# Optimization experiments

Hardware: AMD Instinct MI355X
Metric: run time of the kernel (lower is better)

The kernel has to match this reference:

```python
import jax, jax.numpy as jnp
import numpy as np

N_BATCH, C, H, W = 4, 64, 64, 64


def setup_inputs() -> dict:
    key = jax.random.key(0)
    ks = jax.random.split(key, 8)
    x = jax.random.normal(ks[0], (N_BATCH, C, H, W), dtype=jnp.float32)
    wb = jax.random.normal(ks[1], (C, C), dtype=jnp.float32) * 0.05
    bb = jax.random.normal(ks[2], (C,), dtype=jnp.float32) * 0.05
    wc = jax.random.normal(ks[3], (C, C), dtype=jnp.float32) * 0.05
    bc = jax.random.normal(ks[4], (C,), dtype=jnp.float32) * 0.05
    wd = jax.random.normal(ks[5], (C, C), dtype=jnp.float32) * 0.05
    bd = jax.random.normal(ks[6], (C,), dtype=jnp.float32) * 0.05
    alpha = jax.random.normal(ks[7], (1,), dtype=jnp.float32)
    return {"x": x, "wb": wb, "bb": bb, "wc": wc, "bc": bc,
            "wd": wd, "bd": bd, "alpha": alpha}


def reference(x, wb, bb, wc, bc, wd, bd, alpha):
    n, c, h, w = x.shape
    xf = x.reshape(n, c, h * w)  # (n, c, L)
    # 1x1 convs == per-pixel channel GEMMs
    xb = jnp.einsum('oc,ncl->nol', wb, xf) + bb[None, :, None]  # keys   (n, c, L)
    xc = jnp.einsum('oc,ncl->nol', wc, xf) + bc[None, :, None]  # queries(n, c, L)
    xd = jnp.einsum('oc,ncl->nol', wd, xf) + bd[None, :, None]  # values (n, c, L)
    # attention[i, j] = <xc[:, i], xb[:, j]>, softmax over j
    attention = jnp.einsum('nci,ncj->nij', xc, xb)  # (n, L, L)
    att = jax.nn.softmax(attention, axis=-1)
    # x_o[:, :, i] = sum_j xd[:, :, j] * att[i, j]
    x_o = jnp.einsum('ncj,nij->nci', xd, att).reshape(n, c, h, w)
    return alpha[0] * x_o + x
```

## Files before the change

### kernel.cpp

```cpp
#include <hip/hip_runtime.h>
#include <hip/hip_bf16.h>

typedef unsigned short u16;
typedef unsigned char u8;
typedef unsigned int u32;
typedef long long i64;
typedef __attribute__((ext_vector_type(4))) float f32x4;
typedef __attribute__((ext_vector_type(4))) unsigned int u32x4;

#define L_SEQ 4096
#define NCH 64
#define NBATCH 4
#define NW 8
#define KVSPAN (L_SEQ / NW)
#define QB 32
#define DEFER_THR 4.0f

__device__ inline u16 f2bf(float f) {
    union { float f; u32 u; } v; v.f = f;
    u32 r = v.u + 0x7fffu + ((v.u >> 16) & 1u);
    return (u16)(r >> 16);
}

template <bool WORD>
__device__ inline u32 pk_fp8(float a, float b, u32 old) {
    return (u32)__builtin_amdgcn_cvt_pk_fp8_f32(a, b, (int)old, WORD);
}
__device__ inline u8 fp8_1(float a) {
    return (u8)(__builtin_amdgcn_cvt_pk_fp8_f32(a, a, 0, false) & 0xff);
}

__global__ __launch_bounds__(256) void qkv_kernel(
    const float* __restrict__ x,
    const float* __restrict__ wb, const float* __restrict__ bb,
    const float* __restrict__ wc, const float* __restrict__ bc,
    const float* __restrict__ wd, const float* __restrict__ bd,
    u8* __restrict__ Qp8, u8* __restrict__ Kp8, u8* __restrict__ Vp8)
{
    __shared__ float xs[64][64];
    __shared__ float wl[3][64][65];

    const int nb  = blockIdx.y;
    const int i0  = blockIdx.x * 64;
    const int tid = threadIdx.x;

    const float* xbase = x + (size_t)nb * NCH * L_SEQ + i0;
    #pragma unroll
    for (int rep = 0; rep < 16; ++rep) {
        int idx = rep * 256 + tid;
        int c = idx >> 6, px = idx & 63;
        xs[c][px] = xbase[(size_t)c * L_SEQ + px];
    }
    const float* wsrc[3] = { wb, wc, wd };
    for (int m = 0; m < 3; ++m) {
        #pragma unroll
        for (int rep = 0; rep < 16; ++rep) {
            int idx = rep * 256 + tid;
            wl[m][idx >> 6][idx & 63] = wsrc[m][idx];
        }
    }
    __syncthreads();

    const int co  = tid & 63;
    const int pg  = tid >> 6;
    const int px0 = pg * 16;

    float accB[16], accC[16], accD[16];
    const float biasB = bb[co], biasC = bc[co], biasD = bd[co];
    #pragma unroll
    for (int p = 0; p < 16; ++p) { accB[p] = biasB; accC[p] = biasC; accD[p] = biasD; }

    for (int c = 0; c < 64; ++c) {
        const float wbv = wl[0][co][c];
        const float wcv = wl[1][co][c];
        const float wdv = wl[2][co][c];
        #pragma unroll
        for (int p = 0; p < 16; ++p) {
            const float xv = xs[c][px0 + p];
            accB[p] += wbv * xv;
            accC[p] += wcv * xv;
            accD[p] += wdv * xv;
        }
    }

    const size_t nbase = (size_t)nb * L_SEQ * NCH;
    const int jb     = i0 / 16 + pg;
    const int kbase8 = ((co & 31) >> 3) * 256 + (co >> 5) * 8 + (co & 7);
    const int vbase8 = (i0 >> 6) * 4096 + (co >> 4) * 1024 + (co & 15) * 16
                     + (pg >> 1) * 8 + (pg & 1) * 4;

    #pragma unroll
    for (int p = 0; p < 16; ++p) {
        const int i = i0 + px0 + p;
        Kp8[nbase + jb * 1024 + kbase8 + p * 16] = fp8_1(accB[p]);
        Qp8[nbase + (size_t)i * 64 + co]         = fp8_1(accC[p]);
    }
    #pragma unroll
    for (int pq = 0; pq < 4; ++pq) {
        u32 wv = pk_fp8<false>(accD[pq * 4 + 0], accD[pq * 4 + 1], 0);
        wv     = pk_fp8<true >(accD[pq * 4 + 2], accD[pq * 4 + 3], wv);
        *(u32*)&Vp8[nbase + vbase8 + pq * 256] = wv;
    }
}

__global__ __launch_bounds__(512, 4) void attn_kernel(
    const u8* __restrict__ Qp8, const u8* __restrict__ Kp8,
    const u8* __restrict__ Vp8, const float* __restrict__ x,
    const float* __restrict__ alphap, float* __restrict__ out)
{
    __shared__ float smem[NW][QB * 65];
    __shared__ float mlbuf[NW][QB][2];

    const int nb   = blockIdx.y;
    const int i0   = blockIdx.x * QB;
    const int tid  = threadIdx.x;
    const int w    = tid >> 6;
    const int lane = tid & 63;
    const int lo   = lane & 15;
    const int hi   = lane >> 4;

    i64 qf[2][2];
    #pragma unroll
    for (int qt = 0; qt < 2; ++qt) {
        const u8* qrow = Qp8 + (size_t)(nb * L_SEQ + i0 + qt * 16 + lo) * 64;
        qf[qt][0] = *(const i64*)(qrow + hi * 8);
        qf[qt][1] = *(const i64*)(qrow + 32 + hi * 8);
    }

    const f32x4 zero = { 0.f, 0.f, 0.f, 0.f };
    f32x4 acc_o[2][4];
    #pragma unroll
    for (int qt = 0; qt < 2; ++qt)
        #pragma unroll
        for (int ct = 0; ct < 4; ++ct) acc_o[qt][ct] = zero;
    float m_[2] = { -3.0e38f, -3.0e38f }, l_[2] = { 0.f, 0.f };

    const u8* KpB = Kp8 + (size_t)nb * L_SEQ * NCH;
    const u8* VpB = Vp8 + (size_t)nb * NCH * L_SEQ;

    union F8 { u32 u[2]; i64 ll; };

    #pragma unroll 1
    for (int t = 0; t < KVSPAN / 64; ++t) {
        const int j0 = w * KVSPAN + t * 64;

        f32x4 s[2][4];
        #pragma unroll
        for (int jt = 0; jt < 4; ++jt) {
            const u32x4 kw = *(const u32x4*)(KpB + (size_t)(j0 / 16 + jt) * 1024 + lane * 16);
            F8 k0, k1;
            k0.u[0] = kw[0]; k0.u[1] = kw[1];
            k1.u[0] = kw[2]; k1.u[1] = kw[3];
            #pragma unroll
            for (int qt = 0; qt < 2; ++qt) {
                f32x4 a = zero;
                a = __builtin_amdgcn_mfma_f32_16x16x32_fp8_fp8(k0.ll, qf[qt][0], a, 0, 0, 0);
                a = __builtin_amdgcn_mfma_f32_16x16x32_fp8_fp8(k1.ll, qf[qt][1], a, 0, 0, 0);
                s[qt][jt] = a;
            }
        }

        F8 pf[2][2];
        #pragma unroll
        for (int qt = 0; qt < 2; ++qt) {
            float rm = fmaxf(
                fmaxf(fmaxf(fmaxf(s[qt][0][0], s[qt][0][1]), fmaxf(s[qt][0][2], s[qt][0][3])),
                      fmaxf(fmaxf(s[qt][1][0], s[qt][1][1]), fmaxf(s[qt][1][2], s[qt][1][3]))),
                fmaxf(fmaxf(fmaxf(s[qt][2][0], s[qt][2][1]), fmaxf(s[qt][2][2], s[qt][2][3])),
                      fmaxf(fmaxf(s[qt][3][0], s[qt][3][1]), fmaxf(s[qt][3][2], s[qt][3][3]))));
            rm = fmaxf(rm, __shfl_xor(rm, 16, 64));
            rm = fmaxf(rm, __shfl_xor(rm, 32, 64));

            if (!__all(rm <= m_[qt] + DEFER_THR)) {
                const float mn  = fmaxf(m_[qt], rm);
                const float scl = __expf(m_[qt] - mn);
                l_[qt] *= scl;
                m_[qt] = mn;
                #pragma unroll
                for (int ct = 0; ct < 4; ++ct)
                    #pragma unroll
                    for (int r = 0; r < 4; ++r)
                        acc_o[qt][ct][r] *= scl;
            }
            const float mn = m_[qt];

            float p[4][4];
            float rs = 0.f;
            #pragma unroll
            for (int jt = 0; jt < 4; ++jt)
                #pragma unroll
                for (int r = 0; r < 4; ++r) {
                    p[jt][r] = __expf(s[qt][jt][r] - mn);
                    rs += p[jt][r];
                }
            rs += __shfl_xor(rs, 16, 64);
            rs += __shfl_xor(rs, 32, 64);
            l_[qt] += rs;

            pf[qt][0].u[0] = pk_fp8<true>(p[0][2], p[0][3], pk_fp8<false>(p[0][0], p[0][1], 0));
            pf[qt][0].u[1] = pk_fp8<true>(p[1][2], p[1][3], pk_fp8<false>(p[1][0], p[1][1], 0));
            pf[qt][1].u[0] = pk_fp8<true>(p[2][2], p[2][3], pk_fp8<false>(p[2][0], p[2][1], 0));
            pf[qt][1].u[1] = pk_fp8<true>(p[3][2], p[3][3], pk_fp8<false>(p[3][0], p[3][1], 0));
        }

        #pragma unroll
        for (int ct = 0; ct < 4; ++ct) {
            const u32x4 vw = *(const u32x4*)(VpB + (size_t)(j0 >> 6) * 4096 + ct * 1024 + lane * 16);
            F8 v0, v1;
            v0.u[0] = vw[0]; v0.u[1] = vw[1];
            v1.u[0] = vw[2]; v1.u[1] = vw[3];
            #pragma unroll
            for (int qt = 0; qt < 2; ++qt) {
                acc_o[qt][ct] = __builtin_amdgcn_mfma_f32_16x16x32_fp8_fp8(v0.ll, pf[qt][0].ll, acc_o[qt][ct], 0, 0, 0);
                acc_o[qt][ct] = __builtin_amdgcn_mfma_f32_16x16x32_fp8_fp8(v1.ll, pf[qt][1].ll, acc_o[qt][ct], 0, 0, 0);
            }
        }
    }

    #pragma unroll
    for (int qt = 0; qt < 2; ++qt)
        #pragma unroll
        for (int ct = 0; ct < 4; ++ct)
            #pragma unroll
            for (int r = 0; r < 4; ++r)
                smem[w][(qt * 16 + lo) * 65 + ct * 16 + hi * 4 + r] = acc_o[qt][ct][r];
    if (hi == 0) {
        #pragma unroll
        for (int qt = 0; qt < 2; ++qt) {
            mlbuf[w][qt * 16 + lo][0] = m_[qt];
            mlbuf[w][qt * 16 + lo][1] = l_[qt];
        }
    }
    __syncthreads();

    const int q  = tid & 31;
    const int c0 = (tid >> 5) * 4;

    float gm = -3.0e38f;
    #pragma unroll
    for (int s2 = 0; s2 < NW; ++s2) gm = fmaxf(gm, mlbuf[s2][q][0]);

    float Ls = 0.f, O[4] = { 0.f, 0.f, 0.f, 0.f };
    #pragma unroll
    for (int s2 = 0; s2 < NW; ++s2) {
        const float cf = __expf(mlbuf[s2][q][0] - gm);
        Ls += mlbuf[s2][q][1] * cf;
        #pragma unroll
        for (int k = 0; k < 4; ++k)
            O[k] += smem[s2][q * 65 + c0 + k] * cf;
    }
    const float rl    = __builtin_amdgcn_rcpf(Ls);
    const float alpha = alphap[0];

    #pragma unroll
    for (int k = 0; k < 4; ++k) {
        const size_t idx = ((size_t)(nb * NCH + c0 + k)) * L_SEQ + i0 + q;
        out[idx] = alpha * O[k] * rl + x[idx];
    }
}

extern "C" void kernel_launch(void* const* d_in, const int* in_sizes, int n_in,
                              void* d_out, int out_size, void* d_ws, size_t ws_size,
                              hipStream_t stream) {
    const float* x     = (const float*)d_in[0];
    const float* wb    = (const float*)d_in[1];
    const float* bb    = (const float*)d_in[2];
    const float* wc    = (const float*)d_in[3];
    const float* bc    = (const float*)d_in[4];
    const float* wd    = (const float*)d_in[5];
    const float* bd    = (const float*)d_in[6];
    const float* alpha = (const float*)d_in[7];

    const size_t elems = (size_t)NBATCH * L_SEQ * NCH;
    u8* Qp8 = (u8*)d_ws;
    u8* Kp8 = Qp8 + elems;
    u8* Vp8 = Kp8 + elems;

    qkv_kernel<<<dim3(L_SEQ / 64, NBATCH), 256, 0, stream>>>(
        x, wb, bb, wc, bc, wd, bd, Qp8, Kp8, Vp8);
    attn_kernel<<<dim3(L_SEQ / QB, NBATCH), 512, 0, stream>>>(
        Qp8, Kp8, Vp8, x, alpha, (float*)d_out);
}
```

Measured before the change: 39.97 us.

## Split KV across grid blocks and merge partials in a separate combine kernel

Before, each block's 8 waves split the KV range for a single 32-query tile and merged through shared memory. Now each wave owns its own 32 queries, blocks span 256 queries, and a grid z-dimension of 8 splits the KV range. Each split writes its partial output as bf16 plus its softmax max/sum statistics to workspace. A new combine kernel rescales and sums the partials and then applies alpha and the residual. This lets all 8 waves of a block share K/V tiles through cache, at the cost of an extra launch, global round-trips of the partials, and bf16 rounding of the partial outputs.

Result: slower. 49.55 us (+24.0%).

```diff
diff --git a/kernel.cpp b/kernel.cpp
--- a/kernel.cpp
+++ b/kernel.cpp
@@ -7,20 +7,16 @@
 typedef long long i64;
 typedef __attribute__((ext_vector_type(4))) float f32x4;
 typedef __attribute__((ext_vector_type(4))) unsigned int u32x4;
+typedef __attribute__((ext_vector_type(2))) unsigned int uint2_t;
+typedef __attribute__((ext_vector_type(2))) float float2_t;
 
 #define L_SEQ 4096
 #define NCH 64
 #define NBATCH 4
 #define NW 8
-#define KVSPAN (L_SEQ / NW)
-#define QB 32
+#define SPLITS 8
+#define TPS 8
 #define DEFER_THR 4.0f
-
-__device__ inline u16 f2bf(float f) {
-    union { float f; u32 u; } v; v.f = f;
-    u32 r = v.u + 0x7fffu + ((v.u >> 16) & 1u);
-    return (u16)(r >> 16);
-}
 
 template <bool WORD>
 __device__ inline u32 pk_fp8(float a, float b, u32 old) {
@@ -28,6 +24,11 @@
 }
 __device__ inline u8 fp8_1(float a) {
     return (u8)(__builtin_amdgcn_cvt_pk_fp8_f32(a, a, 0, false) & 0xff);
+}
+__device__ inline u32 cvtpk_bf(float a, float b) {
+    u32 r;
+    asm("v_cvt_pk_bf16_f32 %0, %1, %2" : "=v"(r) : "v"(a), "v"(b));
+    return r;
 }
 
 __global__ __launch_bounds__(256) void qkv_kernel(
@@ -105,24 +106,24 @@
 
 __global__ __launch_bounds__(512, 4) void attn_kernel(
     const u8* __restrict__ Qp8, const u8* __restrict__ Kp8,
-    const u8* __restrict__ Vp8, const float* __restrict__ x,
-    const float* __restrict__ alphap, float* __restrict__ out)
+    const u8* __restrict__ Vp8, u16* __restrict__ Opart,
+    float* __restrict__ mlpart)
 {
-    __shared__ float smem[NW][QB * 65];
-    __shared__ float mlbuf[NW][QB][2];
-
     const int nb   = blockIdx.y;
-    const int i0   = blockIdx.x * QB;
+    const int qb   = blockIdx.x;
+    const int sp   = blockIdx.z;
     const int tid  = threadIdx.x;
     const int w    = tid >> 6;
     const int lane = tid & 63;
     const int lo   = lane & 15;
     const int hi   = lane >> 4;
 
+    const int qbase = qb * 256 + w * 32;
+
     i64 qf[2][2];
     #pragma unroll
     for (int qt = 0; qt < 2; ++qt) {
-        const u8* qrow = Qp8 + (size_t)(nb * L_SEQ + i0 + qt * 16 + lo) * 64;
+        const u8* qrow = Qp8 + (size_t)(nb * L_SEQ + qbase + qt * 16 + lo) * 64;
         qf[qt][0] = *(const i64*)(qrow + hi * 8);
         qf[qt][1] = *(const i64*)(qrow + 32 + hi * 8);
     }
@@ -141,8 +142,8 @@
     union F8 { u32 u[2]; i64 ll; };
 
     #pragma unroll 1
-    for (int t = 0; t < KVSPAN / 64; ++t) {
-        const int j0 = w * KVSPAN + t * 64;
+    for (int t = 0; t < TPS; ++t) {
+        const int j0 = sp * (TPS * 64) + t * 64;
 
         f32x4 s[2][4];
         #pragma unroll
@@ -217,44 +218,67 @@
         }
     }
 
-    #pragma unroll
-    for (int qt = 0; qt < 2; ++qt)
-        #pragma unroll
-        for (int ct = 0; ct < 4; ++ct)
-            #pragma unroll
-            for (int r = 0; r < 4; ++r)
-                smem[w][(qt * 16 + lo) * 65 + ct * 16 + hi * 4 + r] = acc_o[qt][ct][r];
-    if (hi == 0) {
-        #pragma unroll
-        for (int qt = 0; qt < 2; ++qt) {
-            mlbuf[w][qt * 16 + lo][0] = m_[qt];
-            mlbuf[w][qt * 16 + lo][1] = l_[qt];
-        }
-    }
-    __syncthreads();
-
-    const int q  = tid & 31;
-    const int c0 = (tid >> 5) * 4;
-
+    const size_t pb = (size_t)(sp * NBATCH + nb) * L_SEQ;
+    #pragma unroll
+    for (int qt = 0; qt < 2; ++qt) {
+        const int q = qbase + qt * 16 + lo;
+        #pragma unroll
+        for (int ct = 0; ct < 4; ++ct) {
+            uint2_t pk;
+            pk[0] = cvtpk_bf(acc_o[qt][ct][0], acc_o[qt][ct][1]);
+            pk[1] = cvtpk_bf(acc_o[qt][ct][2], acc_o[qt][ct][3]);
+            *(uint2_t*)&Opart[(pb + q) * 64 + ct * 16 + hi * 4] = pk;
+        }
+        if (hi == 0) {
+            float2_t ml; ml[0] = m_[qt]; ml[1] = l_[qt];
+            *(float2_t*)&mlpart[(pb + q) * 2] = ml;
+        }
+    }
+}
+
+__global__ __launch_bounds__(256) void combine_kernel(
+    const u16* __restrict__ Opart, const float* __restrict__ mlpart,
+    const float* __restrict__ x, const float* __restrict__ alphap,
+    float* __restrict__ out)
+{
+    const int gid = blockIdx.x * 256 + threadIdx.x;
+    const int cg  = gid & 7;
+    const int q   = (gid >> 3) & (L_SEQ - 1);
+    const int nb  = gid >> 15;
+    const int c0  = cg * 8;
+
+    float ms[SPLITS], ls[SPLITS];
     float gm = -3.0e38f;
     #pragma unroll
-    for (int s2 = 0; s2 < NW; ++s2) gm = fmaxf(gm, mlbuf[s2][q][0]);
-
-    float Ls = 0.f, O[4] = { 0.f, 0.f, 0.f, 0.f };
-    #pragma unroll
-    for (int s2 = 0; s2 < NW; ++s2) {
-        const float cf = __expf(mlbuf[s2][q][0] - gm);
-        Ls += mlbuf[s2][q][1] * cf;
-        #pragma unroll
-        for (int k = 0; k < 4; ++k)
-            O[k] += smem[s2][q * 65 + c0 + k] * cf;
-    }
+    for (int s = 0; s < SPLITS; ++s) {
+        const float2_t ml = *(const float2_t*)&mlpart[((size_t)(s * NBATCH + nb) * L_SEQ + q) * 2];
+        ms[s] = ml[0]; ls[s] = ml[1];
+        gm = fmaxf(gm, ml[0]);
+    }
+
+    float Ls = 0.f, O[8];
+    #pragma unroll
+    for (int k = 0; k < 8; ++k) O[k] = 0.f;
+    #pragma unroll
+    for (int s = 0; s < SPLITS; ++s) {
+        const float cf = __expf(ms[s] - gm);
+        Ls += ls[s] * cf;
+        u32x4 pv = *(const u32x4*)&Opart[((size_t)(s * NBATCH + nb) * L_SEQ + q) * 64 + c0];
+        #pragma unroll
+        for (int k2 = 0; k2 < 4; ++k2) {
+            union { u32 u; float f; } a, b;
+            a.u = (pv[k2] & 0xffffu) << 16;
+            b.u = pv[k2] & 0xffff0000u;
+            O[k2 * 2]     += cf * a.f;
+            O[k2 * 2 + 1] += cf * b.f;
+        }
+    }
+
     const float rl    = __builtin_amdgcn_rcpf(Ls);
     const float alpha = alphap[0];
-
-    #pragma unroll
-    for (int k = 0; k < 4; ++k) {
-        const size_t idx = ((size_t)(nb * NCH + c0 + k)) * L_SEQ + i0 + q;
+    #pragma unroll
+    for (int k = 0; k < 8; ++k) {
+        const size_t idx = ((size_t)(nb * NCH + c0 + k)) * L_SEQ + q;
         out[idx] = alpha * O[k] * rl + x[idx];
     }
 }
@@ -275,9 +299,13 @@
     u8* Qp8 = (u8*)d_ws;
     u8* Kp8 = Qp8 + elems;
     u8* Vp8 = Kp8 + elems;
+    u16* Opart = (u16*)(Vp8 + elems);
+    float* mlpart = (float*)(Opart + (size_t)SPLITS * elems);
 
     qkv_kernel<<<dim3(L_SEQ / 64, NBATCH), 256, 0, stream>>>(
         x, wb, bb, wc, bc, wd, bd, Qp8, Kp8, Vp8);
-    attn_kernel<<<dim3(L_SEQ / QB, NBATCH), 512, 0, stream>>>(
-        Qp8, Kp8, Vp8, x, alpha, (float*)d_out);
-}
+    attn_kernel<<<dim3(L_SEQ / 256, NBATCH, SPLITS), 512, 0, stream>>>(
+        Qp8, Kp8, Vp8, Opart, mlpart);
+    combine_kernel<<<dim3(NBATCH * L_SEQ * 8 / 256), 256, 0, stream>>>(
+        Opart, mlpart, x, alpha, (float*)d_out);
+}
```
